# Kernel optimization log

Hardware: AMD Instinct MI355X
Metric: run time of the kernel (lower is better)

Reference implementation:

```python
import jax, jax.numpy as jnp
import numpy as np

ALPHA = 0.25  # sparsity init kwarg


def setup_inputs() -> dict:
    key = jax.random.key(0)
    x = jax.random.uniform(key, (32, 256, 256, 16), dtype=jnp.float32)
    return {"x": x}


def reference(x):
    # Original TF code loops over every pixel i in H*W, slicing (B,1,C) and
    # calling force_sparsity, where p = reduce_mean over the WHOLE slice
    # (batch AND channel). Vectorized: p has shape (H, W).
    p = jnp.mean(x, axis=(0, 3))            # (H, W) per-pixel mean over B,C
    p_b = p[None, :, :, None]                # broadcast to (1, H, W, 1)
    beta = (1.0 - ALPHA) / (1.0 - p_b)
    le = p_b >= ALPHA                        # branch selector per pixel
    out = jnp.where(le,
                    x * ALPHA / p_b,
                    1.0 - beta * (1.0 - x))
    return out
```

## Files before the change

kernel.cpp:

```cpp
#include <hip/hip_runtime.h>


#define ALPHA 0.25f

typedef float v4f __attribute__((ext_vector_type(4)));

__global__ __launch_bounds__(256) void rescale_prob_mask_kernel(
    const float* __restrict__ x, float* __restrict__ out) {
  constexpr long F4_PER_B = 256L * 256 * 16 / 4;

  const int tile = blockIdx.x;
  const int h    = tile >> 4;
  const int w0   = (tile & 15) << 4;
  const long tile_base_f4 = (((long)h * 256 + w0) * 16) >> 2;

  const int t    = threadIdx.x;
  const int lane = t & 63;
  const int wv   = t >> 6;

  const float4* __restrict__ p4 =
      (const float4*)x + tile_base_f4 + (long)wv * F4_PER_B + lane;
  float* __restrict__ obase =
      (float*)out + 4 * (tile_base_f4 + (long)wv * F4_PER_B + lane);

  float4 v[8];
#pragma unroll
  for (int k = 0; k < 8; ++k) {
    v[k] = p4[(long)k * 4 * F4_PER_B];
  }

  float s = 0.0f;
#pragma unroll
  for (int k = 0; k < 8; ++k) {
    s += (v[k].x + v[k].y) + (v[k].z + v[k].w);
  }
  s += __shfl_xor(s, 1);
  s += __shfl_xor(s, 2);

  __shared__ float lds[4][16];
  const int wp = lane >> 2;
  if ((lane & 3) == 0) lds[wv][wp] = s;
  __syncthreads();
  const float psum = (lds[0][wp] + lds[1][wp]) + (lds[2][wp] + lds[3][wp]);
  const float p = psum * (1.0f / 512.0f);

  float a, d;
  if (p >= ALPHA) {
    a = ALPHA / p;
    d = 0.0f;
  } else {
    const float beta = (1.0f - ALPHA) / (1.0f - p);
    a = beta;
    d = 1.0f - beta;
  }

#pragma unroll
  for (int k = 0; k < 8; ++k) {
    asm volatile("" : "+v"(v[k].x), "+v"(v[k].y), "+v"(v[k].z), "+v"(v[k].w));
  }

#pragma unroll
  for (int k = 0; k < 8; ++k) {
    v4f r;
    r.x = fmaf(a, v[k].x, d);
    r.y = fmaf(a, v[k].y, d);
    r.z = fmaf(a, v[k].z, d);
    r.w = fmaf(a, v[k].w, d);
    __builtin_nontemporal_store(
        r, (v4f*)(obase + (long)k * 4 * F4_PER_B * 4));
  }
}

extern "C" void kernel_launch(void* const* d_in, const int* in_sizes, int n_in,
                              void* d_out, int out_size, void* d_ws, size_t ws_size,
                              hipStream_t stream) {
  const float* x = (const float*)d_in[0];
  float* out = (float*)d_out;
  rescale_prob_mask_kernel<<<dim3(4096), dim3(256), 0, stream>>>(x, out);
}
```

Before: 238.8 us.

## Stage tile loads via global_load_lds and reduce per-pixel mean with shuffles

```diff
diff --git a/kernel.cpp b/kernel.cpp
--- a/kernel.cpp
+++ b/kernel.cpp
@@ -7,42 +7,44 @@
 
 __global__ __launch_bounds__(256) void rescale_prob_mask_kernel(
     const float* __restrict__ x, float* __restrict__ out) {
-  constexpr long F4_PER_B = 256L * 256 * 16 / 4;
+  constexpr int ELEM_PER_B = 256 * 256 * 16;
+
+  __shared__ float lds[32][256];
 
   const int tile = blockIdx.x;
   const int h    = tile >> 4;
   const int w0   = (tile & 15) << 4;
-  const long tile_base_f4 = (((long)h * 256 + w0) * 16) >> 2;
+  const long tile_base_f = ((long)h * 256 + w0) * 16;
 
-  const int t    = threadIdx.x;
-  const int lane = t & 63;
-  const int wv   = t >> 6;
+  const int t  = threadIdx.x;
+  const int l  = t & 63;
+  const int wv = t >> 6;
 
-  const float4* __restrict__ p4 =
-      (const float4*)x + tile_base_f4 + (long)wv * F4_PER_B + lane;
-  float* __restrict__ obase =
-      (float*)out + 4 * (tile_base_f4 + (long)wv * F4_PER_B + lane);
-
-  float4 v[8];
 #pragma unroll
   for (int k = 0; k < 8; ++k) {
-    v[k] = p4[(long)k * 4 * F4_PER_B];
+    const int b = 4 * k + wv;
+    const float* src = x + tile_base_f + (long)b * ELEM_PER_B + l * 4;
+    __builtin_amdgcn_global_load_lds(
+        (const __attribute__((address_space(1))) unsigned int*)src,
+        (__attribute__((address_space(3))) unsigned int*)&lds[b][0],
+        16, 0, 0);
   }
+  __syncthreads();
 
+  const int j = l & 15;
+  float4 v[8];
   float s = 0.0f;
 #pragma unroll
   for (int k = 0; k < 8; ++k) {
+    const int r = 4 * k + (l >> 4);
+    v[k] = *(const float4*)&lds[r][wv * 64 + j * 4];
     s += (v[k].x + v[k].y) + (v[k].z + v[k].w);
   }
   s += __shfl_xor(s, 1);
   s += __shfl_xor(s, 2);
-
-  __shared__ float lds[4][16];
-  const int wp = lane >> 2;
-  if ((lane & 3) == 0) lds[wv][wp] = s;
-  __syncthreads();
-  const float psum = (lds[0][wp] + lds[1][wp]) + (lds[2][wp] + lds[3][wp]);
-  const float p = psum * (1.0f / 512.0f);
+  s += __shfl_xor(s, 16);
+  s += __shfl_xor(s, 32);
+  const float p = s * (1.0f / 512.0f);
 
   float a, d;
   if (p >= ALPHA) {
@@ -56,18 +58,14 @@
 
 #pragma unroll
   for (int k = 0; k < 8; ++k) {
-    asm volatile("" : "+v"(v[k].x), "+v"(v[k].y), "+v"(v[k].z), "+v"(v[k].w));
-  }
-
-#pragma unroll
-  for (int k = 0; k < 8; ++k) {
-    v4f r;
-    r.x = fmaf(a, v[k].x, d);
-    r.y = fmaf(a, v[k].y, d);
-    r.z = fmaf(a, v[k].z, d);
-    r.w = fmaf(a, v[k].w, d);
-    __builtin_nontemporal_store(
-        r, (v4f*)(obase + (long)k * 4 * F4_PER_B * 4));
+    const int r = 4 * k + (l >> 4);
+    v4f o;
+    o.x = fmaf(a, v[k].x, d);
+    o.y = fmaf(a, v[k].y, d);
+    o.z = fmaf(a, v[k].z, d);
+    o.w = fmaf(a, v[k].w, d);
+    float* dst = out + tile_base_f + (long)r * ELEM_PER_B + (wv * 16 + j) * 4;
+    __builtin_nontemporal_store(o, (v4f*)dst);
   }
 }
 
```

Result: no change. 241.1 us (+1.0%).
